# Optimization experiments

Hardware: AMD Instinct MI355X
Metric: run time of the kernel (lower is better)

Reference implementation:

```python
import jax, jax.numpy as jnp
import numpy as np

B, T, IMG, PS, D, DEPTH, NH = 1, 8, 224, 16, 768, 12, 12
HP = IMG // PS
NP = HP * HP          # 196 patches per frame
N = NP + 1            # +1 cls token per frame
DH = D // NH
MLP = 4 * D
SCALE = DH ** -0.5


def _ln(x, g, b):
    mu = x.mean(-1, keepdims=True)
    var = ((x - mu) ** 2).mean(-1, keepdims=True)
    return (x - mu) / jnp.sqrt(var + 1e-5) * g + b


def _forward(x, W_patch, b_patch, cls_token, pos_embed,
             ln1_g, ln1_b, qkv_w, qkv_b, proj_w, proj_b,
             ln2_g, ln2_b, fc1_w, fc1_b, fc2_w, fc2_b, lnf_g, lnf_b):
    Bc = x.shape[0]
    # --- patch embed (Conv3d k=(1,ps,ps), stride=(1,ps,ps) == per-frame patch matmul) ---
    p = x.reshape(Bc, T, 3, HP, PS, HP, PS).transpose(0, 1, 3, 5, 2, 4, 6)
    p = p.reshape(Bc, T, NP, 3 * PS * PS)
    emb = p @ W_patch.T + b_patch                     # [B,T,NP,D] (correct layout)
    # replicate torch flatten(3)/transpose(1,2)/reshape axis scramble:
    emb = jnp.swapaxes(emb, 2, 3).reshape(Bc, T, NP, D)
    cls = jnp.broadcast_to(cls_token.reshape(1, 1, 1, D), (Bc, T, 1, D))
    h = jnp.concatenate([cls, emb], axis=2) + pos_embed.reshape(1, 1, N, D)
    h = h.reshape(Bc, T * N, D)

    for i in range(DEPTH):
        # --- attention ---
        a = _ln(h, ln1_g[i], ln1_b[i])
        qkv = (a @ qkv_w[i] + qkv_b[i]).reshape(Bc, T * N, 3, NH, DH)
        q, k, v = (jnp.transpose(qkv[:, :, j], (0, 2, 1, 3)) for j in range(3))  # [B,H,S,dh]
        if i % 2 == 0:  # divided space-time
            qf = q.reshape(Bc, NH, T, N, DH)
            kf = k.reshape(Bc, NH, T, N, DH)
            vf = v.reshape(Bc, NH, T, N, DH)
            q_t = qf.mean(3, keepdims=True)           # [B,H,T,1,dh]
            k_t = kf.mean(3, keepdims=True)
            v_t = vf.mean(3, keepdims=True)
            attn_t = jax.nn.softmax(jnp.einsum('bhtqd,bhtkd->bhtqk', q_t, k_t) * SCALE, -1)
            x_t = jnp.einsum('bhtqk,bhtkd->bhtqd', attn_t, v_t)[:, :, :, 0]  # [B,H,T,dh]
            attn_s = jax.nn.softmax(jnp.einsum('bhtqd,bhtkd->bhtqk', qf, kf) * SCALE, -1)
            x_s = jnp.einsum('bhtqk,bhtkd->bhtqd', attn_s, vf)               # [B,H,T,N,dh]
            o = (x_s + x_t[:, :, :, None, :]).reshape(Bc, NH, T * N, DH)
        else:  # joint space-time
            attn = jax.nn.softmax(jnp.einsum('bhqd,bhkd->bhqk', q, k) * SCALE, -1)
            o = jnp.einsum('bhqk,bhkd->bhqd', attn, v)
        o = jnp.transpose(o, (0, 2, 1, 3)).reshape(Bc, T * N, D)
        h = h + (o @ proj_w[i] + proj_b[i])
        # --- mlp ---
        m = _ln(h, ln2_g[i], ln2_b[i])
        m = jax.nn.gelu(m @ fc1_w[i] + fc1_b[i], approximate=False)
        h = h + (m @ fc2_w[i] + fc2_b[i])

    return _ln(h, lnf_g, lnf_b).reshape(Bc, T, N, D)


def setup_inputs() -> dict:
    key = jax.random.key(0)
    ks = jax.random.split(key, 12)
    s = 0.02
    return {
        'x': jax.random.normal(ks[0], (B, T, 3, IMG, IMG), jnp.float32),
        'W_patch': jax.random.normal(ks[1], (D, 3 * PS * PS), jnp.float32) * s,
        'b_patch': jnp.zeros((D,), jnp.float32),
        'cls_token': jax.random.normal(ks[2], (1, 1, D), jnp.float32) * s,
        'pos_embed': jax.random.normal(ks[3], (1, N, D), jnp.float32) * s,
        'ln1_g': jnp.ones((DEPTH, D), jnp.float32),
        'ln1_b': jnp.zeros((DEPTH, D), jnp.float32),
        'qkv_w': jax.random.normal(ks[4], (DEPTH, D, 3 * D), jnp.float32) * s,
        'qkv_b': jnp.zeros((DEPTH, 3 * D), jnp.float32),
        'proj_w': jax.random.normal(ks[5], (DEPTH, D, D), jnp.float32) * s,
        'proj_b': jnp.zeros((DEPTH, D), jnp.float32),
        'ln2_g': jnp.ones((DEPTH, D), jnp.float32),
        'ln2_b': jnp.zeros((DEPTH, D), jnp.float32),
        'fc1_w': jax.random.normal(ks[6], (DEPTH, D, MLP), jnp.float32) * s,
        'fc1_b': jnp.zeros((DEPTH, MLP), jnp.float32),
        'fc2_w': jax.random.normal(ks[7], (DEPTH, MLP, D), jnp.float32) * s,
        'fc2_b': jnp.zeros((DEPTH, D), jnp.float32),
        'lnf_g': jnp.ones((D,), jnp.float32),
        'lnf_b': jnp.zeros((D,), jnp.float32),
    }


def reference(x, W_patch, b_patch, cls_token, pos_embed,
              ln1_g, ln1_b, qkv_w, qkv_b, proj_w, proj_b,
              ln2_g, ln2_b, fc1_w, fc1_b, fc2_w, fc2_b, lnf_g, lnf_b):
    return _forward(x, W_patch, b_patch, cls_token, pos_embed,
                    ln1_g, ln1_b, qkv_w, qkv_b, proj_w, proj_b,
                    ln2_g, ln2_b, fc1_w, fc1_b, fc2_w, fc2_b, lnf_g, lnf_b)
```

## Files before the change

### kernel.cpp

```cpp
#include <hip/hip_runtime.h>
#include <math.h>

#define Dm 768
#define Tn 8
#define Nn 197
#define Sn 1576
#define MLPn 3072
#define NPn 196
#define MPAD 1664

typedef unsigned short u16;
typedef __bf16 bf16x8 __attribute__((ext_vector_type(8)));
typedef float f32x4 __attribute__((ext_vector_type(4)));
typedef unsigned int u32x4 __attribute__((ext_vector_type(4)));
typedef u16 u16x8 __attribute__((ext_vector_type(8)));
typedef u16 u16x4 __attribute__((ext_vector_type(4)));

__device__ inline u16 f2bf(float f) {
    union { float f; unsigned u; } v; v.f = f;
    unsigned r = v.u + 0x7fffu + ((v.u >> 16) & 1u);
    return (u16)(r >> 16);
}
__device__ inline float bf2f(u16 v) {
    union { unsigned u; float f; } x; x.u = ((unsigned)v) << 16; return x.f;
}

__device__ __forceinline__ void gl_lds16(const u16* __restrict__ g, u16* l) {
    __builtin_amdgcn_global_load_lds((const __attribute__((address_space(1))) void*)g,
                                     (__attribute__((address_space(3))) void*)l,
                                     16, 0, 0);
}

__global__ __launch_bounds__(256) void im2col_k(const float* __restrict__ x, u16* __restrict__ P) {
    int idx = blockIdx.x * 256 + threadIdx.x;
    if (idx >= 1568 * 768) return;
    int c = idx % 768, r = idx / 768;
    int p = r % 196, t = r / 196;
    int hp = p / 14, wp = p % 14;
    int ch = c / 256, rem = c % 256, py = rem / 16, px = rem % 16;
    P[idx] = f2bf(x[((t * 3 + ch) * 224 + hp * 16 + py) * 224 + wp * 16 + px]);
}

__global__ __launch_bounds__(256) void cvt_k(const float* __restrict__ s, u16* __restrict__ d, int n) {
    int i = blockIdx.x * 256 + threadIdx.x;
    if (i < n) d[i] = f2bf(s[i]);
}

__global__ __launch_bounds__(256) void cvtT_layer_k(const float* __restrict__ qw, const float* __restrict__ pw,
                                                    const float* __restrict__ f1w, const float* __restrict__ f2w,
                                                    u16* __restrict__ Wq, u16* __restrict__ Wp,
                                                    u16* __restrict__ W1, u16* __restrict__ W2) {
    __shared__ float tile[32][33];
    int bid = blockIdx.x;
    const float* src; u16* dst; int K, N, k0, n0;
    if (bid < 1728)      { src = qw;  dst = Wq; K = 768;  N = 2304; int r = bid;        k0 = (r / 72) * 32; n0 = (r % 72) * 32; }
    else if (bid < 2304) { src = pw;  dst = Wp; K = 768;  N = 768;  int r = bid - 1728; k0 = (r / 24) * 32; n0 = (r % 24) * 32; }
    else if (bid < 4608) { src = f1w; dst = W1; K = 768;  N = 3072; int r = bid - 2304; k0 = (r / 96) * 32; n0 = (r % 96) * 32; }
    else                 { src = f2w; dst = W2; K = 3072; N = 768;  int r = bid - 4608; k0 = (r / 24) * 32; n0 = (r % 24) * 32; }
    int tx = threadIdx.x & 31, ty = threadIdx.x >> 5;
#pragma unroll
    for (int i = 0; i < 4; ++i) tile[ty + 8 * i][tx] = src[(size_t)(k0 + ty + 8 * i) * N + n0 + tx];
    __syncthreads();
#pragma unroll
    for (int i = 0; i < 4; ++i) dst[(size_t)(n0 + ty + 8 * i) * K + k0 + tx] = f2bf(tile[tx][ty + 8 * i]);
}

__global__ __launch_bounds__(256) void build_h_k(const float* __restrict__ emb, const float* __restrict__ cls,
                                                 const float* __restrict__ pos, float* __restrict__ h) {
    int idx = blockIdx.x * 256 + threadIdx.x;
    if (idx >= Sn * Dm) return;
    int d = idx % Dm, s = idx / Dm;
    int t = s / Nn, r = s % Nn;
    float v;
    if (r == 0) v = cls[d];
    else {
        int f = (r - 1) * Dm + d;
        int p = f % NPn, dd = f / NPn;
        v = emb[(size_t)(t * NPn + p) * Dm + dd];
    }
    h[idx] = v + pos[r * Dm + d];
}

template <typename OutT>
__global__ __launch_bounds__(256) void ln_k(const float* __restrict__ X, const float* __restrict__ g,
                                            const float* __restrict__ bta, OutT* __restrict__ Y) {
    int row = blockIdx.x;
    const float* x = X + (size_t)row * Dm;
    float s = 0.f, s2 = 0.f;
#pragma unroll
    for (int q = 0; q < 3; ++q) {
        float v = x[threadIdx.x + q * 256];
        s += v; s2 += v * v;
    }
#pragma unroll
    for (int off = 1; off < 64; off <<= 1) {
        s  += __shfl_xor(s,  off);
        s2 += __shfl_xor(s2, off);
    }
    __shared__ float red[8];
    int wv = threadIdx.x >> 6;
    if ((threadIdx.x & 63) == 0) { red[wv * 2] = s; red[wv * 2 + 1] = s2; }
    __syncthreads();
    s  = red[0] + red[2] + red[4] + red[6];
    s2 = red[1] + red[3] + red[5] + red[7];
    float mu  = s * (1.f / 768.f);
    float var = s2 * (1.f / 768.f) - mu * mu;
    float rstd = rsqrtf(var + 1e-5f);
#pragma unroll
    for (int q = 0; q < 3; ++q) {
        int i = threadIdx.x + q * 256;
        float v = (x[i] - mu) * rstd * g[i] + bta[i];
        if constexpr (sizeof(OutT) == 2) Y[(size_t)row * Dm + i] = f2bf(v);
        else                             Y[(size_t)row * Dm + i] = v;
    }
}

__global__ __launch_bounds__(256) void mgemm_k(const u16* __restrict__ A, const u16* __restrict__ Bt,
                                               float* __restrict__ Cp, int N, int Kfull, int Kc) {
    __shared__ __align__(16) u16 As[2 * 4096];
    __shared__ __align__(16) u16 Bs[2 * 4096];
    int split = blockIdx.z;
    A  += split * Kc;
    Bt += split * Kc;
    Cp += (size_t)split * MPAD * N;
    int tid = threadIdx.x;
    int lane = tid & 63, w = tid >> 6;
    int wm = w & 1, wn = w >> 1;
    int m0 = blockIdx.y * 128, n0 = blockIdx.x * 128;
    f32x4 acc[4][4] = {};
    int c0 = tid, c1 = tid + 256;
    int ar0 = ((c0 >> 6) << 4) + (c0 & 15), ac0 = ((c0 >> 4) & 3) << 3;
    int ar1 = ((c1 >> 6) << 4) + (c1 & 15), ac1 = ((c1 >> 4) & 3) << 3;
    const u16* Arow0 = A  + (size_t)(m0 + ar0) * Kfull + ac0;
    const u16* Arow1 = A  + (size_t)(m0 + ar1) * Kfull + ac1;
    const u16* Brow0 = Bt + (size_t)(n0 + ar0) * Kfull + ac0;
    const u16* Brow1 = Bt + (size_t)(n0 + ar1) * Kfull + ac1;
    auto STAGE = [&](int buf, int k0) {
        int bo = buf << 12;
        gl_lds16(Arow0 + k0, As + bo + (w * 64) * 8);
        gl_lds16(Arow1 + k0, As + bo + (256 + w * 64) * 8);
        gl_lds16(Brow0 + k0, Bs + bo + (w * 64) * 8);
        gl_lds16(Brow1 + k0, Bs + bo + (256 + w * 64) * 8);
    };
    STAGE(0, 0);
    asm volatile("s_waitcnt vmcnt(0)" ::: "memory");
    __builtin_amdgcn_s_barrier();
    int cur = 0;
    for (int k0 = 0; k0 < Kc; k0 += 32) {
        if (k0 + 32 < Kc) STAGE(cur ^ 1, k0 + 32);
        const u16* Ab = As + (cur << 12);
        const u16* Bb = Bs + (cur << 12);
        bf16x8 af[4], bfr[4];
#pragma unroll
        for (int i = 0; i < 4; ++i) {
            af[i]  = *(const bf16x8*)(Ab + (((wm * 4 + i) * 64 + lane) << 3));
            bfr[i] = *(const bf16x8*)(Bb + (((wn * 4 + i) * 64 + lane) << 3));
        }
#pragma unroll
        for (int mi = 0; mi < 4; ++mi)
#pragma unroll
            for (int ni = 0; ni < 4; ++ni)
                acc[mi][ni] = __builtin_amdgcn_mfma_f32_16x16x32_bf16(af[mi], bfr[ni], acc[mi][ni], 0, 0, 0);
        asm volatile("s_waitcnt vmcnt(0)" ::: "memory");
        __builtin_amdgcn_s_barrier();
        cur ^= 1;
    }
    int rbase = (lane >> 4) << 2, cl = lane & 15;
#pragma unroll
    for (int mi = 0; mi < 4; ++mi)
#pragma unroll
        for (int r = 0; r < 4; ++r) {
            int gm = m0 + wm * 64 + mi * 16 + rbase + r;
#pragma unroll
            for (int ni = 0; ni < 4; ++ni) {
                int gn = n0 + wn * 64 + ni * 16 + cl;
                Cp[(size_t)gm * N + gn] = acc[mi][ni][r];
            }
        }
}

template <bool GELU_ACT>
__global__ __launch_bounds__(256) void mgemm_fused_k(const u16* __restrict__ A, const u16* __restrict__ Bt,
                                                     const float* __restrict__ bias, u16* __restrict__ out,
                                                     int N, int Kfull, int Mout) {
    __shared__ __align__(16) u16 As[2 * 64 * 32];
    __shared__ __align__(16) u16 Bs[2 * 128 * 32];
    int tid = threadIdx.x;
    int lane = tid & 63, w = tid >> 6;
    int wm = w & 1, wn = w >> 1;
    int m0 = blockIdx.y * 64, n0 = blockIdx.x * 128;
    f32x4 acc[2][4] = {};
    int ca = tid;
    int ar = ((ca >> 6) << 4) + (ca & 15), ac = ((ca >> 4) & 3) << 3;
    const u16* Arow = A + (size_t)(m0 + ar) * Kfull + ac;
    int cb1 = tid + 256;
    int br1 = ((cb1 >> 6) << 4) + (cb1 & 15), bc1 = ((cb1 >> 4) & 3) << 3;
    const u16* Brow0 = Bt + (size_t)(n0 + ar) * Kfull + ac;
    const u16* Brow1 = Bt + (size_t)(n0 + br1) * Kfull + bc1;
    auto STAGE = [&](int buf, int k0) {
        gl_lds16(Arow + k0, As + (buf << 11) + (w * 64) * 8);
        gl_lds16(Brow0 + k0, Bs + (buf << 12) + (w * 64) * 8);
        gl_lds16(Brow1 + k0, Bs + (buf << 12) + (256 + w * 64) * 8);
    };
    STAGE(0, 0);
    asm volatile("s_waitcnt vmcnt(0)" ::: "memory");
    __builtin_amdgcn_s_barrier();
    int cur = 0;
    for (int k0 = 0; k0 < Kfull; k0 += 32) {
        if (k0 + 32 < Kfull) STAGE(cur ^ 1, k0 + 32);
        const u16* Ab = As + (cur << 11);
        const u16* Bb = Bs + (cur << 12);
        bf16x8 af[2], bfr[4];
#pragma unroll
        for (int i = 0; i < 2; ++i) af[i]  = *(const bf16x8*)(Ab + (((wm * 2 + i) * 64 + lane) << 3));
#pragma unroll
        for (int j = 0; j < 4; ++j) bfr[j] = *(const bf16x8*)(Bb + (((wn * 4 + j) * 64 + lane) << 3));
#pragma unroll
        for (int mi = 0; mi < 2; ++mi)
#pragma unroll
            for (int ni = 0; ni < 4; ++ni)
                acc[mi][ni] = __builtin_amdgcn_mfma_f32_16x16x32_bf16(af[mi], bfr[ni], acc[mi][ni], 0, 0, 0);
        asm volatile("s_waitcnt vmcnt(0)" ::: "memory");
        __builtin_amdgcn_s_barrier();
        cur ^= 1;
    }
    int rbase = (lane >> 4) << 2, cl = lane & 15;
#pragma unroll
    for (int mi = 0; mi < 2; ++mi)
#pragma unroll
        for (int r = 0; r < 4; ++r) {
            int gm = m0 + wm * 32 + mi * 16 + rbase + r;
            if (gm < Mout) {
#pragma unroll
                for (int ni = 0; ni < 4; ++ni) {
                    int gn = n0 + wn * 64 + ni * 16 + cl;
                    float v = acc[mi][ni][r] + bias[gn];
                    if (GELU_ACT) v = 0.5f * v * (1.f + erff(v * 0.7071067811865476f));
                    out[(size_t)gm * N + gn] = f2bf(v);
                }
            }
        }
}

__global__ __launch_bounds__(256) void ep_k(const float* __restrict__ Cp, const float* __restrict__ bias,
                                            float* __restrict__ out, int N, int S) {
    int row = blockIdx.y;
    int n = blockIdx.x * 1024 + threadIdx.x * 4;
    if (n >= N) return;
    size_t off = (size_t)row * N + n;
    f32x4 acc = *(const f32x4*)(Cp + off);
    for (int s = 1; s < S; ++s)
        acc += *(const f32x4*)(Cp + (size_t)s * MPAD * N + off);
    acc += *(const f32x4*)(bias + n);
    *(f32x4*)(out + off) = acc;
}

template <bool FINALOUT>
__global__ __launch_bounds__(256) void ep_ln_k(const float* __restrict__ Cp, const float* __restrict__ bias,
                                               float* __restrict__ h, const float* __restrict__ g,
                                               const float* __restrict__ bta, void* __restrict__ lnout, int S) {
    int row = blockIdx.x;
    int t = threadIdx.x;
    float v[3];
    float s = 0.f, s2 = 0.f;
#pragma unroll
    for (int q = 0; q < 3; ++q) {
        int i = t + q * 256;
        size_t off = (size_t)row * Dm + i;
        float a = Cp[off];
        for (int sp = 1; sp < S; ++sp) a += Cp[(size_t)sp * MPAD * Dm + off];
        a += bias[i] + h[off];
        h[off] = a;
        v[q] = a; s += a; s2 += a * a;
    }
#pragma unroll
    for (int off = 1; off < 64; off <<= 1) {
        s  += __shfl_xor(s,  off);
        s2 += __shfl_xor(s2, off);
    }
    __shared__ float red[8];
    int wv = t >> 6;
    if ((t & 63) == 0) { red[wv * 2] = s; red[wv * 2 + 1] = s2; }
    __syncthreads();
    s  = red[0] + red[2] + red[4] + red[6];
    s2 = red[1] + red[3] + red[5] + red[7];
    float mu  = s * (1.f / 768.f);
    float var = s2 * (1.f / 768.f) - mu * mu;
    float rstd = rsqrtf(var + 1e-5f);
#pragma unroll
    for (int q = 0; q < 3; ++q) {
        int i = t + q * 256;
        float y = (v[q] - mu) * rstd * g[i] + bta[i];
        if constexpr (FINALOUT) ((float*)lnout)[(size_t)row * Dm + i] = y;
        else                    ((u16*)lnout)[(size_t)row * Dm + i] = f2bf(y);
    }
}

__global__ __launch_bounds__(256) void vmean_k(const u16* __restrict__ qkv, float* __restrict__ vm) {
    int g = blockIdx.x;
    int h = g >> 3, t = g & 7;
    int d = threadIdx.x & 63, part = threadIdx.x >> 6;
    float s = 0.f;
    for (int n = part; n < Nn; n += 4)
        s += bf2f(qkv[(size_t)(t * Nn + n) * 2304 + 1536 + h * 64 + d]);
    __shared__ float red[256];
    red[threadIdx.x] = s;
    __syncthreads();
    if (part == 0) vm[g * 64 + d] = (red[d] + red[64 + d] + red[128 + d] + red[192 + d]) * (1.f / 197.f);
}

__global__ __launch_bounds__(256) void attn_mfma_k(const u16* __restrict__ qkv, float* __restrict__ Ou,
                                                   float* __restrict__ ml, const float* __restrict__ vm,
                                                   u16* __restrict__ ob, int even, int nsplit,
                                                   int NG, int Sq, int fuse) {
    __shared__ __align__(16) u16 Ks[64 * 64];
    __shared__ __align__(16) u16 Vt[64 * 64];
    __shared__ __align__(16) u16 Ps[4 * 32 * 64];
    int g = blockIdx.y;
    int h, sbase;
    if (even) { h = g >> 3; sbase = (g & 7) * Nn; } else { h = g; sbase = 0; }
    int split = blockIdx.z;
    int chunk = (Sq + nsplit - 1) / nsplit;
    int kbeg = split * chunk, kend = min(Sq, kbeg + chunk);
    int tid = threadIdx.x, lane = tid & 63, w = tid >> 6;
    int quad = lane >> 4, l15 = lane & 15;
    int q0w = blockIdx.x * 128 + w * 32;
    u16* Pw = Ps + w * 2048;

    bf16x8 aq[2][2];
#pragma unroll
    for (int mb = 0; mb < 2; ++mb) {
        int qidx = q0w + mb * 16 + l15; if (qidx >= Sq) qidx = Sq - 1;
        const u16* qp = qkv + (size_t)(sbase + qidx) * 2304 + h * 64;
#pragma unroll
        for (int ks = 0; ks < 2; ++ks)
            aq[mb][ks] = *(const bf16x8*)(qp + ks * 32 + quad * 8);
    }
    f32x4 acc_o[2][4] = {};
    float m_run[2][4], l_run[2][4];
#pragma unroll
    for (int mb = 0; mb < 2; ++mb)
#pragma unroll
        for (int r = 0; r < 4; ++r) { m_run[mb][r] = -INFINITY; l_run[mb][r] = 0.f; }

    for (int kt = kbeg; kt < kend; kt += 64) {
        int cnt = kend - kt; if (cnt > 64) cnt = 64;
        {
            int dc = tid & 7;
#pragma unroll
            for (int p = 0; p < 2; ++p) {
                int row = (tid >> 3) + 32 * p;
                u32x4 kd = {};
                if (row < cnt) kd = *(const u32x4*)(qkv + (size_t)(sbase + kt + row) * 2304 + 768 + h * 64 + dc * 8);
                *(u32x4*)(Ks + row * 64 + ((dc ^ (row & 7)) << 3)) = kd;
            }
        }
        {
            int d = (tid & 31) * 2, kc = tid >> 5;
            u16x8 lo, hi;
#pragma unroll
            for (int i = 0; i < 8; ++i) {
                int key = kc * 8 + i;
                unsigned t = 0;
                if (key < cnt) t = *(const unsigned*)(qkv + (size_t)(sbase + kt + key) * 2304 + 1536 + h * 64 + d);
                lo[i] = (u16)(t & 0xffffu); hi[i] = (u16)(t >> 16);
            }
            *(u16x8*)(Vt + d * 64 + ((kc ^ (d & 7)) << 3)) = lo;
            *(u16x8*)(Vt + (d + 1) * 64 + ((kc ^ ((d + 1) & 7)) << 3)) = hi;
        }
        __syncthreads();
        f32x4 acc_s[2][4] = {};
#pragma unroll
        for (int ni = 0; ni < 4; ++ni) {
            int key = l15 + ni * 16;
#pragma unroll
            for (int ks = 0; ks < 2; ++ks) {
                bf16x8 bk = *(const bf16x8*)(Ks + key * 64 + ((((ks << 2) + quad) ^ (key & 7)) << 3));
                acc_s[0][ni] = __builtin_amdgcn_mfma_f32_16x16x32_bf16(aq[0][ks], bk, acc_s[0][ni], 0, 0, 0);
                acc_s[1][ni] = __builtin_amdgcn_mfma_f32_16x16x32_bf16(aq[1][ks], bk, acc_s[1][ni], 0, 0, 0);
            }
        }
#pragma unroll
        for (int mb = 0; mb < 2; ++mb) {
#pragma unroll
            for (int ni = 0; ni < 4; ++ni) {
                int keyabs = kt + l15 + ni * 16;
#pragma unroll
                for (int r = 0; r < 4; ++r) {
                    float sv = acc_s[mb][ni][r] * 0.125f;
                    if (keyabs >= kend) sv = -1e30f;
                    acc_s[mb][ni][r] = sv;
                }
            }
#pragma unroll
            for (int r = 0; r < 4; ++r) {
                float mx = fmaxf(fmaxf(acc_s[mb][0][r], acc_s[mb][1][r]), fmaxf(acc_s[mb][2][r], acc_s[mb][3][r]));
                mx = fmaxf(mx, __shfl_xor(mx, 1));
                mx = fmaxf(mx, __shfl_xor(mx, 2));
                mx = fmaxf(mx, __shfl_xor(mx, 4));
                mx = fmaxf(mx, __shfl_xor(mx, 8));
                float mnew = fmaxf(m_run[mb][r], mx);
                float pv[4], ps = 0.f;
#pragma unroll
                for (int ni = 0; ni < 4; ++ni) { pv[ni] = __expf(acc_s[mb][ni][r] - mnew); ps += pv[ni]; }
                ps += __shfl_xor(ps, 1);
                ps += __shfl_xor(ps, 2);
                ps += __shfl_xor(ps, 4);
                ps += __shfl_xor(ps, 8);
                float alpha = __expf(m_run[mb][r] - mnew);
                l_run[mb][r] = l_run[mb][r] * alpha + ps;
                m_run[mb][r] = mnew;
#pragma unroll
                for (int ni = 0; ni < 4; ++ni) acc_o[mb][ni][r] *= alpha;
                int prow = mb * 16 + quad * 4 + r;
#pragma unroll
                for (int ni = 0; ni < 4; ++ni) {
                    int key = l15 + ni * 16;
                    Pw[prow * 64 + (((key >> 3) ^ (prow & 7)) << 3) + (key & 7)] = f2bf(pv[ni]);
                }
            }
        }
        bf16x8 ap[2][2];
#pragma unroll
        for (int mb = 0; mb < 2; ++mb)
#pragma unroll
            for (int ks = 0; ks < 2; ++ks)
                ap[mb][ks] = *(const bf16x8*)(Pw + (mb * 16 + l15) * 64 + ((((ks << 2) + quad) ^ (l15 & 7)) << 3));
#pragma unroll
        for (int ni = 0; ni < 4; ++ni) {
            int d = l15 + ni * 16;
#pragma unroll
            for (int ks = 0; ks < 2; ++ks) {
                bf16x8 bv = *(const bf16x8*)(Vt + d * 64 + ((((ks << 2) + quad) ^ (d & 7)) << 3));
                acc_o[0][ni] = __builtin_amdgcn_mfma_f32_16x16x32_bf16(ap[0][ks], bv, acc_o[0][ni], 0, 0, 0);
                acc_o[1][ni] = __builtin_amdgcn_mfma_f32_16x16x32_bf16(ap[1][ks], bv, acc_o[1][ni], 0, 0, 0);
            }
        }
        __syncthreads();
    }
    if (fuse) {
#pragma unroll
        for (int mb = 0; mb < 2; ++mb)
#pragma unroll
            for (int r = 0; r < 4; ++r) {
                int q = q0w + mb * 16 + quad * 4 + r;
                if (q < Sq) {
                    float inv = 1.f / l_run[mb][r];
                    u16* op = ob + (size_t)(sbase + q) * Dm + h * 64;
#pragma unroll
                    for (int ni = 0; ni < 4; ++ni) {
                        int d = l15 + ni * 16;
                        op[d] = f2bf(acc_o[mb][ni][r] * inv + vm[g * 64 + d]);
                    }
                }
            }
    } else {
        size_t gb = ((size_t)split * NG + g) * Sq;
#pragma unroll
        for (int mb = 0; mb < 2; ++mb)
#pragma unroll
            for (int r = 0; r < 4; ++r) {
                int q = q0w + mb * 16 + quad * 4 + r;
                if (q < Sq) {
                    float* op = Ou + (gb + q) * 64;
#pragma unroll
                    for (int ni = 0; ni < 4; ++ni) op[l15 + ni * 16] = acc_o[mb][ni][r];
                    if (l15 == 0) {
                        ml[(gb + q) * 2]     = m_run[mb][r];
                        ml[(gb + q) * 2 + 1] = l_run[mb][r];
                    }
                }
            }
    }
}

__global__ __launch_bounds__(256) void comb_k(const float* __restrict__ Ou, const float* __restrict__ ml,
                                              u16* __restrict__ ob, int nsplit, int NG, int Sq) {
    int g = blockIdx.y;
    int q = blockIdx.x * 4 + (threadIdx.x >> 6);
    int d = threadIdx.x & 63;
    if (q >= Sq) return;
    int h = g, sbase = 0;
    float M = -INFINITY;
    for (int s = 0; s < nsplit; ++s) M = fmaxf(M, ml[(((size_t)s * NG + g) * Sq + q) * 2]);
    float num = 0.f, den = 0.f;
    for (int s = 0; s < nsplit; ++s) {
        size_t base = ((size_t)s * NG + g) * Sq + q;
        float wgt = __expf(ml[base * 2] - M);
        den += wgt * ml[base * 2 + 1];
        num += wgt * Ou[base * 64 + d];
    }
    float o = num / den;
    ob[(size_t)(sbase + q) * Dm + h * 64 + d] = f2bf(o);
}

extern "C" void kernel_launch(void* const* d_in, const int* in_sizes, int n_in,
                              void* d_out, int out_size, void* d_ws, size_t ws_size,
                              hipStream_t stream) {
    (void)in_sizes; (void)n_in; (void)out_size; (void)ws_size;
    const float* x       = (const float*)d_in[0];
    const float* W_patch = (const float*)d_in[1];
    const float* b_patch = (const float*)d_in[2];
    const float* cls     = (const float*)d_in[3];
    const float* pos     = (const float*)d_in[4];
    const float* ln1_g   = (const float*)d_in[5];
    const float* ln1_b   = (const float*)d_in[6];
    const float* qkv_w   = (const float*)d_in[7];
    const float* qkv_b   = (const float*)d_in[8];
    const float* proj_w  = (const float*)d_in[9];
    const float* proj_b  = (const float*)d_in[10];
    const float* ln2_g   = (const float*)d_in[11];
    const float* ln2_b   = (const float*)d_in[12];
    const float* fc1_w   = (const float*)d_in[13];
    const float* fc1_b   = (const float*)d_in[14];
    const float* fc2_w   = (const float*)d_in[15];
    const float* fc2_b   = (const float*)d_in[16];
    const float* lnf_g   = (const float*)d_in[17];
    const float* lnf_b   = (const float*)d_in[18];

    char* base = (char*)d_ws;
    auto alloc = [&](size_t bytes) { void* p = base; base += (bytes + 255) & ~(size_t)255; return p; };
    u16*   P    = (u16*)  alloc((size_t)MPAD * 768 * 2);
    u16*   Wq   = (u16*)  alloc((size_t)2304 * 768 * 2);
    u16*   Wp   = (u16*)  alloc((size_t)768 * 768 * 2);
    u16*   W1   = (u16*)  alloc((size_t)3072 * 768 * 2);
    u16*   W2   = (u16*)  alloc((size_t)768 * 3072 * 2);
    float* emb  = (float*)alloc((size_t)1568 * 768 * 4);
    float* h    = (float*)alloc((size_t)Sn * Dm * 4);
    u16*   a    = (u16*)  alloc((size_t)MPAD * 768 * 2);
    u16*   qkvb = (u16*)  alloc((size_t)Sn * 2304 * 2);
    u16*   ob   = (u16*)  alloc((size_t)MPAD * 768 * 2);
    u16*   mb   = (u16*)  alloc((size_t)MPAD * 3072 * 2);
    float* vm   = (float*)alloc((size_t)96 * 64 * 4);
    float* Ou   = (float*)alloc((size_t)3 * 12 * Sn * 64 * 4);
    float* ml   = (float*)alloc((size_t)3 * 12 * Sn * 2 * 4);
    float* Cp   = (float*)alloc((size_t)4 * MPAD * 768 * 4);

    im2col_k<<<(1568 * 768 + 255) / 256, 256, 0, stream>>>(x, P);
    cvt_k<<<(768 * 768 + 255) / 256, 256, 0, stream>>>(W_patch, Wp, 768 * 768);
    mgemm_k<<<dim3(6, 13, 3), 256, 0, stream>>>(P, Wp, Cp, 768, 768, 256);
    ep_k<<<dim3(1, 1568), 256, 0, stream>>>(Cp, b_patch, emb, 768, 3);
    build_h_k<<<(Sn * Dm + 255) / 256, 256, 0, stream>>>(emb, cls, pos, h);
    ln_k<u16><<<Sn, 256, 0, stream>>>(h, ln1_g, ln1_b, a);

    for (int i = 0; i < 12; ++i) {
        cvtT_layer_k<<<6912, 256, 0, stream>>>(
            qkv_w + (size_t)i * 768 * 2304, proj_w + (size_t)i * 768 * 768,
            fc1_w + (size_t)i * 768 * 3072, fc2_w + (size_t)i * 3072 * 768,
            Wq, Wp, W1, W2);
        mgemm_fused_k<false><<<dim3(18, 26), 256, 0, stream>>>(a, Wq, qkv_b + i * 2304, qkvb, 2304, 768, Sn);
        if ((i & 1) == 0) {
            vmean_k<<<96, 256, 0, stream>>>(qkvb, vm);
            attn_mfma_k<<<dim3(2, 96, 1), 256, 0, stream>>>(qkvb, Ou, ml, vm, ob, 1, 1, 96, Nn, 1);
        } else {
            attn_mfma_k<<<dim3(13, 12, 3), 256, 0, stream>>>(qkvb, Ou, ml, vm, ob, 0, 3, 12, Sn, 0);
            comb_k<<<dim3(394, 12), 256, 0, stream>>>(Ou, ml, ob, 3, 12, Sn);
        }
        mgemm_k<<<dim3(6, 13, 4), 256, 0, stream>>>(ob, Wp, Cp, 768, 768, 192);
        ep_ln_k<false><<<Sn, 256, 0, stream>>>(Cp, proj_b + i * Dm, h, ln2_g + i * Dm, ln2_b + i * Dm, a, 4);
        mgemm_fused_k<true><<<dim3(24, 26), 256, 0, stream>>>(a, W1, fc1_b + i * MLPn, mb, 3072, 768, Sn);
        mgemm_k<<<dim3(6, 13, 4), 256, 0, stream>>>(mb, W2, Cp, 768, 3072, 768);
        if (i < 11)
            ep_ln_k<false><<<Sn, 256, 0, stream>>>(Cp, fc2_b + i * Dm, h, ln1_g + (i + 1) * Dm, ln1_b + (i + 1) * Dm, a, 4);
        else
            ep_ln_k<true><<<Sn, 256, 0, stream>>>(Cp, fc2_b + i * Dm, h, lnf_g, lnf_b, d_out, 4);
    }
}
```

Before: 2.279 ms.

## Batch all-layer weight conversion and triple-buffer GEMM LDS pipelines

All 12 layers' weights are converted and transposed to bf16 in one large launch up front instead of one launch per layer, which removes 11 launches and the per-layer serialization between weight conversion and GEMM. Both GEMM kernels move from a double-buffered to a triple-buffered LDS pipeline that prefetches two k-tiles ahead and waits with partial vmcnt counts instead of draining all loads every iteration. This costs 12x more workspace for weights and 50% more LDS per block, which may lower occupancy.

```diff
diff --git a/kernel.cpp b/kernel.cpp
--- a/kernel.cpp
+++ b/kernel.cpp
@@ -46,11 +46,20 @@
     if (i < n) d[i] = f2bf(s[i]);
 }
 
-__global__ __launch_bounds__(256) void cvtT_layer_k(const float* __restrict__ qw, const float* __restrict__ pw,
-                                                    const float* __restrict__ f1w, const float* __restrict__ f2w,
-                                                    u16* __restrict__ Wq, u16* __restrict__ Wp,
-                                                    u16* __restrict__ W1, u16* __restrict__ W2) {
+__global__ __launch_bounds__(256) void cvtT_all_k(const float* __restrict__ qw_, const float* __restrict__ pw_,
+                                                  const float* __restrict__ f1w_, const float* __restrict__ f2w_,
+                                                  u16* __restrict__ Wq_, u16* __restrict__ Wp_,
+                                                  u16* __restrict__ W1_, u16* __restrict__ W2_) {
     __shared__ float tile[32][33];
+    int layer = blockIdx.y;
+    const float* qw  = qw_  + (size_t)layer * 768 * 2304;
+    const float* pw  = pw_  + (size_t)layer * 768 * 768;
+    const float* f1w = f1w_ + (size_t)layer * 768 * 3072;
+    const float* f2w = f2w_ + (size_t)layer * 3072 * 768;
+    u16* Wq = Wq_ + (size_t)layer * 2304 * 768;
+    u16* Wp = Wp_ + (size_t)layer * 768 * 768;
+    u16* W1 = W1_ + (size_t)layer * 3072 * 768;
+    u16* W2 = W2_ + (size_t)layer * 768 * 3072;
     int bid = blockIdx.x;
     const float* src; u16* dst; int K, N, k0, n0;
     if (bid < 1728)      { src = qw;  dst = Wq; K = 768;  N = 2304; int r = bid;        k0 = (r / 72) * 32; n0 = (r % 72) * 32; }
@@ -117,8 +126,8 @@
 
 __global__ __launch_bounds__(256) void mgemm_k(const u16* __restrict__ A, const u16* __restrict__ Bt,
                                                float* __restrict__ Cp, int N, int Kfull, int Kc) {
-    __shared__ __align__(16) u16 As[2 * 4096];
-    __shared__ __align__(16) u16 Bs[2 * 4096];
+    __shared__ __align__(16) u16 As[3 * 4096];
+    __shared__ __align__(16) u16 Bs[3 * 4096];
     int split = blockIdx.z;
     A  += split * Kc;
     Bt += split * Kc;
@@ -136,20 +145,25 @@
     const u16* Brow0 = Bt + (size_t)(n0 + ar0) * Kfull + ac0;
     const u16* Brow1 = Bt + (size_t)(n0 + ar1) * Kfull + ac1;
     auto STAGE = [&](int buf, int k0) {
-        int bo = buf << 12;
+        int bo = buf * 4096;
         gl_lds16(Arow0 + k0, As + bo + (w * 64) * 8);
         gl_lds16(Arow1 + k0, As + bo + (256 + w * 64) * 8);
         gl_lds16(Brow0 + k0, Bs + bo + (w * 64) * 8);
         gl_lds16(Brow1 + k0, Bs + bo + (256 + w * 64) * 8);
     };
+    int nt = Kc >> 5;
     STAGE(0, 0);
-    asm volatile("s_waitcnt vmcnt(0)" ::: "memory");
-    __builtin_amdgcn_s_barrier();
-    int cur = 0;
-    for (int k0 = 0; k0 < Kc; k0 += 32) {
-        if (k0 + 32 < Kc) STAGE(cur ^ 1, k0 + 32);
-        const u16* Ab = As + (cur << 12);
-        const u16* Bb = Bs + (cur << 12);
+    STAGE(1, 32);
+    int buf = 0;
+    for (int t = 0; t < nt; ++t) {
+        if (t + 2 < nt) { int sb = buf + 2; if (sb >= 3) sb -= 3; STAGE(sb, (t + 2) * 32); }
+        int ahead = nt - 1 - t;
+        if (ahead >= 2)      asm volatile("s_waitcnt vmcnt(8)" ::: "memory");
+        else if (ahead == 1) asm volatile("s_waitcnt vmcnt(4)" ::: "memory");
+        else                 asm volatile("s_waitcnt vmcnt(0)" ::: "memory");
+        __builtin_amdgcn_s_barrier();
+        const u16* Ab = As + buf * 4096;
+        const u16* Bb = Bs + buf * 4096;
         bf16x8 af[4], bfr[4];
 #pragma unroll
         for (int i = 0; i < 4; ++i) {
@@ -161,9 +175,9 @@
 #pragma unroll
             for (int ni = 0; ni < 4; ++ni)
                 acc[mi][ni] = __builtin_amdgcn_mfma_f32_16x16x32_bf16(af[mi], bfr[ni], acc[mi][ni], 0, 0, 0);
-        asm volatile("s_waitcnt vmcnt(0)" ::: "memory");
+        asm volatile("" ::: "memory");
         __builtin_amdgcn_s_barrier();
-        cur ^= 1;
+        buf = (buf == 2) ? 0 : buf + 1;
     }
     int rbase = (lane >> 4) << 2, cl = lane & 15;
 #pragma unroll
@@ -183,8 +197,8 @@
 __global__ __launch_bounds__(256) void mgemm_fused_k(const u16* __restrict__ A, const u16* __restrict__ Bt,
                                                      const float* __restrict__ bias, u16* __restrict__ out,
                                                      int N, int Kfull, int Mout) {
-    __shared__ __align__(16) u16 As[2 * 64 * 32];
-    __shared__ __align__(16) u16 Bs[2 * 128 * 32];
+    __shared__ __align__(16) u16 As[3 * 64 * 32];
+    __shared__ __align__(16) u16 Bs[3 * 128 * 32];
     int tid = threadIdx.x;
     int lane = tid & 63, w = tid >> 6;
     int wm = w & 1, wn = w >> 1;
@@ -198,18 +212,23 @@
     const u16* Brow0 = Bt + (size_t)(n0 + ar) * Kfull + ac;
     const u16* Brow1 = Bt + (size_t)(n0 + br1) * Kfull + bc1;
     auto STAGE = [&](int buf, int k0) {
-        gl_lds16(Arow + k0, As + (buf << 11) + (w * 64) * 8);
-        gl_lds16(Brow0 + k0, Bs + (buf << 12) + (w * 64) * 8);
-        gl_lds16(Brow1 + k0, Bs + (buf << 12) + (256 + w * 64) * 8);
+        gl_lds16(Arow + k0, As + buf * 2048 + (w * 64) * 8);
+        gl_lds16(Brow0 + k0, Bs + buf * 4096 + (w * 64) * 8);
+        gl_lds16(Brow1 + k0, Bs + buf * 4096 + (256 + w * 64) * 8);
     };
+    int nt = Kfull >> 5;
     STAGE(0, 0);
-    asm volatile("s_waitcnt vmcnt(0)" ::: "memory");
-    __builtin_amdgcn_s_barrier();
-    int cur = 0;
-    for (int k0 = 0; k0 < Kfull; k0 += 32) {
-        if (k0 + 32 < Kfull) STAGE(cur ^ 1, k0 + 32);
-        const u16* Ab = As + (cur << 11);
-        const u16* Bb = Bs + (cur << 12);
+    STAGE(1, 32);
+    int buf = 0;
+    for (int t = 0; t < nt; ++t) {
+        if (t + 2 < nt) { int sb = buf + 2; if (sb >= 3) sb -= 3; STAGE(sb, (t + 2) * 32); }
+        int ahead = nt - 1 - t;
+        if (ahead >= 2)      asm volatile("s_waitcnt vmcnt(6)" ::: "memory");
+        else if (ahead == 1) asm volatile("s_waitcnt vmcnt(3)" ::: "memory");
+        else                 asm volatile("s_waitcnt vmcnt(0)" ::: "memory");
+        __builtin_amdgcn_s_barrier();
+        const u16* Ab = As + buf * 2048;
+        const u16* Bb = Bs + buf * 4096;
         bf16x8 af[2], bfr[4];
 #pragma unroll
         for (int i = 0; i < 2; ++i) af[i]  = *(const bf16x8*)(Ab + (((wm * 2 + i) * 64 + lane) << 3));
@@ -220,9 +239,9 @@
 #pragma unroll
             for (int ni = 0; ni < 4; ++ni)
                 acc[mi][ni] = __builtin_amdgcn_mfma_f32_16x16x32_bf16(af[mi], bfr[ni], acc[mi][ni], 0, 0, 0);
-        asm volatile("s_waitcnt vmcnt(0)" ::: "memory");
+        asm volatile("" ::: "memory");
         __builtin_amdgcn_s_barrier();
-        cur ^= 1;
+        buf = (buf == 2) ? 0 : buf + 1;
     }
     int rbase = (lane >> 4) << 2, cl = lane & 15;
 #pragma unroll
@@ -521,10 +540,11 @@
     char* base = (char*)d_ws;
     auto alloc = [&](size_t bytes) { void* p = base; base += (bytes + 255) & ~(size_t)255; return p; };
     u16*   P    = (u16*)  alloc((size_t)MPAD * 768 * 2);
-    u16*   Wq   = (u16*)  alloc((size_t)2304 * 768 * 2);
-    u16*   Wp   = (u16*)  alloc((size_t)768 * 768 * 2);
-    u16*   W1   = (u16*)  alloc((size_t)3072 * 768 * 2);
-    u16*   W2   = (u16*)  alloc((size_t)768 * 3072 * 2);
+    u16*   Wpe  = (u16*)  alloc((size_t)768 * 768 * 2);
+    u16*   Wq   = (u16*)  alloc((size_t)12 * 2304 * 768 * 2);
+    u16*   Wp   = (u16*)  alloc((size_t)12 * 768 * 768 * 2);
+    u16*   W1   = (u16*)  alloc((size_t)12 * 3072 * 768 * 2);
+    u16*   W2   = (u16*)  alloc((size_t)12 * 768 * 3072 * 2);
     float* emb  = (float*)alloc((size_t)1568 * 768 * 4);
     float* h    = (float*)alloc((size_t)Sn * Dm * 4);
     u16*   a    = (u16*)  alloc((size_t)MPAD * 768 * 2);
@@ -536,19 +556,20 @@
     float* ml   = (float*)alloc((size_t)3 * 12 * Sn * 2 * 4);
     float* Cp   = (float*)alloc((size_t)4 * MPAD * 768 * 4);
 
+    cvtT_all_k<<<dim3(6912, 12), 256, 0, stream>>>(qkv_w, proj_w, fc1_w, fc2_w, Wq, Wp, W1, W2);
     im2col_k<<<(1568 * 768 + 255) / 256, 256, 0, stream>>>(x, P);
-    cvt_k<<<(768 * 768 + 255) / 256, 256, 0, stream>>>(W_patch, Wp, 768 * 768);
-    mgemm_k<<<dim3(6, 13, 3), 256, 0, stream>>>(P, Wp, Cp, 768, 768, 256);
+    cvt_k<<<(768 * 768 + 255) / 256, 256, 0, stream>>>(W_patch, Wpe, 768 * 768);
+    mgemm_k<<<dim3(6, 13, 3), 256, 0, stream>>>(P, Wpe, Cp, 768, 768, 256);
     ep_k<<<dim3(1, 1568), 256, 0, stream>>>(Cp, b_patch, emb, 768, 3);
     build_h_k<<<(Sn * Dm + 255) / 256, 256, 0, stream>>>(emb, cls, pos, h);
     ln_k<u16><<<Sn, 256, 0, stream>>>(h, ln1_g, ln1_b, a);
 
     for (int i = 0; i < 12; ++i) {
-        cvtT_layer_k<<<6912, 256, 0, stream>>>(
-            qkv_w + (size_t)i * 768 * 2304, proj_w + (size_t)i * 768 * 768,
-            fc1_w + (size_t)i * 768 * 3072, fc2_w + (size_t)i * 3072 * 768,
-            Wq, Wp, W1, W2);
-        mgemm_fused_k<false><<<dim3(18, 26), 256, 0, stream>>>(a, Wq, qkv_b + i * 2304, qkvb, 2304, 768, Sn);
+        const u16* Wqi = Wq + (size_t)i * 2304 * 768;
+        const u16* Wpi = Wp + (size_t)i * 768 * 768;
+        const u16* W1i = W1 + (size_t)i * 3072 * 768;
+        const u16* W2i = W2 + (size_t)i * 768 * 3072;
+        mgemm_fused_k<false><<<dim3(18, 26), 256, 0, stream>>>(a, Wqi, qkv_b + i * 2304, qkvb, 2304, 768, Sn);
         if ((i & 1) == 0) {
             vmean_k<<<96, 256, 0, stream>>>(qkvb, vm);
             attn_mfma_k<<<dim3(2, 96, 1), 256, 0, stream>>>(qkvb, Ou, ml, vm, ob, 1, 1, 96, Nn, 1);
@@ -556,10 +577,10 @@
             attn_mfma_k<<<dim3(13, 12, 3), 256, 0, stream>>>(qkvb, Ou, ml, vm, ob, 0, 3, 12, Sn, 0);
             comb_k<<<dim3(394, 12), 256, 0, stream>>>(Ou, ml, ob, 3, 12, Sn);
         }
-        mgemm_k<<<dim3(6, 13, 4), 256, 0, stream>>>(ob, Wp, Cp, 768, 768, 192);
+        mgemm_k<<<dim3(6, 13, 4), 256, 0, stream>>>(ob, Wpi, Cp, 768, 768, 192);
         ep_ln_k<false><<<Sn, 256, 0, stream>>>(Cp, proj_b + i * Dm, h, ln2_g + i * Dm, ln2_b + i * Dm, a, 4);
-        mgemm_fused_k<true><<<dim3(24, 26), 256, 0, stream>>>(a, W1, fc1_b + i * MLPn, mb, 3072, 768, Sn);
-        mgemm_k<<<dim3(6, 13, 4), 256, 0, stream>>>(mb, W2, Cp, 768, 3072, 768);
+        mgemm_fused_k<true><<<dim3(24, 26), 256, 0, stream>>>(a, W1i, fc1_b + i * MLPn, mb, 3072, 768, Sn);
+        mgemm_k<<<dim3(6, 13, 4), 256, 0, stream>>>(mb, W2i, Cp, 768, 3072, 768);
         if (i < 11)
             ep_ln_k<false><<<Sn, 256, 0, stream>>>(Cp, fc2_b + i * Dm, h, ln1_g + (i + 1) * Dm, ln1_b + (i + 1) * Dm, a, 4);
         else
```

After: 2.302 ms. About the same (+1.0%).
